# Performance work log

Measured on AMD Instinct MI355X. Metric: run time of the kernel, lower is better.

Reference implementation:

```python
import jax, jax.numpy as jnp
import numpy as np

B, N, M, D0, D, H, KW = 2, 512, 512, 1024, 100, 50, 7
K_SLOPE, X0_SIG = 20.0, 0.5  # LogisticActivation(x0=0.5, k=20), k not trained


def setup_inputs() -> dict:
    key = jax.random.key(0)
    ks = jax.random.split(key, 8)
    s = lambda k, shp: jax.random.normal(k, shp, jnp.float32) * 0.05
    return {
        "x0": jax.random.normal(ks[0], (B, N, D0), jnp.float32),
        "x1": jax.random.normal(ks[1], (B, M, D0), jnp.float32),
        "W_proj": s(ks[2], (D0, D)),
        "b_proj": jnp.zeros((D,), jnp.float32),
        "W_hid": s(ks[3], (2 * D, H)),
        "b_hid": jnp.zeros((H,), jnp.float32),
        "conv_w": s(ks[4], (1, H, KW, KW)),  # OIHW
        "conv_b": jnp.zeros((1,), jnp.float32),
        "theta": jnp.array([0.5], jnp.float32),
        "lambda_": jnp.array([0.3], jnp.float32),
        "gamma": jnp.array([0.2], jnp.float32),
    }


def reference(x0, x1, W_proj, b_proj, W_hid, b_hid, conv_w, conv_b, theta, lambda_, gamma):
    # --- embedding: FullyConnectedEmbed (Linear + ReLU) ---
    e0 = jax.nn.relu(x0 @ W_proj + b_proj)  # [B,N,D]
    e1 = jax.nn.relu(x1 @ W_proj + b_proj)  # [B,M,D]
    # --- contact: broadcast features -> 1x1 conv -> 7x7 conv -> sigmoid ---
    diff = jnp.abs(e0[:, :, None, :] - e1[:, None, :, :])   # [B,N,M,D]
    mul = e0[:, :, None, :] * e1[:, None, :, :]             # [B,N,M,D]
    Z = jnp.concatenate([diff, mul], axis=-1)               # [B,N,M,2D]
    Hh = jax.nn.relu(jnp.einsum('bnmc,ch->bhnm', Z, W_hid) + b_hid[None, :, None, None])
    C = jax.lax.conv_general_dilated(Hh, conv_w, (1, 1), 'SAME')
    C = jax.nn.sigmoid(C + conv_b[None, :, None, None])     # [B,1,N,M]
    # --- weighting matrix W (do_w=True) ---
    i = jnp.arange(N, dtype=jnp.float32)
    j = jnp.arange(M, dtype=jnp.float32)
    a = -jnp.square((i + 1 - (N + 1) / 2) / (-(N + 1) / 2))
    b = -jnp.square((j + 1 - (M + 1) / 2) / (-(M + 1) / 2))
    a = jnp.exp(lambda_ * a)                                 # [N]
    b = jnp.exp(lambda_ * b)                                 # [M]
    W = (1 - theta[0]) * (a[:, None] * b[None, :]) + theta[0]
    yhat = C * W                                             # [B,1,N,M]
    # --- global pooling: mean/var threshold + ratio ---
    mu = jnp.mean(yhat, axis=(1, 2, 3), keepdims=True)
    sigma = jnp.var(yhat, axis=(1, 2, 3), ddof=1, keepdims=True)  # torch.var is unbiased
    Q = jax.nn.relu(yhat - mu - gamma[0] * sigma)
    phat = jnp.sum(Q, axis=(1, 2, 3)) / (jnp.sum(jnp.sign(Q), axis=(1, 2, 3)) + 1)
    # --- LogisticActivation ---
    return jnp.clip(1.0 / (1.0 + jnp.exp(-K_SLOPE * (phat - X0_SIG))), 0.0, 1.0)  # [B]
```

## Files before the change

### kernel.cpp

```cpp
#include <hip/hip_runtime.h>
#include <hip/hip_bf16.h>

static constexpr int Bc   = 2;
static constexpr int Nc   = 512;
static constexpr int Mc   = 512;
static constexpr int D0c  = 1024;
static constexpr int Dc   = 100;
static constexpr int Hc   = 50;
static constexpr long long NMc = (long long)Nc * Mc;

__global__ __launch_bounds__(512) void k_embed(
    const float* __restrict__ x0, const float* __restrict__ x1,
    const float* __restrict__ Wp, const float* __restrict__ bp,
    float* __restrict__ e0, float* __restrict__ e1)
{
  __shared__ float xs[8][1024];
  const int t   = threadIdx.x;
  const int rg0 = blockIdx.x * 8;

  #pragma unroll
  for (int i = 0; i < 4; ++i) {
    const int idx = i*512 + t;
    const int r   = idx >> 8;
    const int c4  = idx & 255;
    const int rgs = rg0 + r;
    const float* src = (rgs < Bc*Nc) ? (x0 + (size_t)rgs * D0c)
                                     : (x1 + (size_t)(rgs - Bc*Nc) * D0c);
    *(float4*)&xs[r][c4*4] = *(const float4*)&src[c4*4];
  }
  __syncthreads();

  const int c = t & 127;
  const int q = t >> 7;
  if (c < Dc) {
    const int row0 = q*2, row1 = q*2 + 1;
    float acc0 = 0.f, acc1 = 0.f;
    for (int k = 0; k < D0c; k += 8) {
      float w[8];
      #pragma unroll
      for (int u = 0; u < 8; ++u) w[u] = Wp[(k+u)*Dc + c];
      const float4 xa0 = *(const float4*)&xs[row0][k];
      const float4 xb0 = *(const float4*)&xs[row0][k+4];
      const float4 xa1 = *(const float4*)&xs[row1][k];
      const float4 xb1 = *(const float4*)&xs[row1][k+4];
      acc0 = fmaf(xa0.x, w[0], acc0); acc1 = fmaf(xa1.x, w[0], acc1);
      acc0 = fmaf(xa0.y, w[1], acc0); acc1 = fmaf(xa1.y, w[1], acc1);
      acc0 = fmaf(xa0.z, w[2], acc0); acc1 = fmaf(xa1.z, w[2], acc1);
      acc0 = fmaf(xa0.w, w[3], acc0); acc1 = fmaf(xa1.w, w[3], acc1);
      acc0 = fmaf(xb0.x, w[4], acc0); acc1 = fmaf(xb1.x, w[4], acc1);
      acc0 = fmaf(xb0.y, w[5], acc0); acc1 = fmaf(xb1.y, w[5], acc1);
      acc0 = fmaf(xb0.z, w[6], acc0); acc1 = fmaf(xb1.z, w[6], acc1);
      acc0 = fmaf(xb0.w, w[7], acc0); acc1 = fmaf(xb1.w, w[7], acc1);
    }
    const float bias = bp[c];
    {
      const int rg = rg0 + row0;
      const float v = fmaxf(acc0 + bias, 0.f);
      if (rg < Bc*Nc) e0[(size_t)rg*Dc + c] = v;
      else            e1[(size_t)(rg - Bc*Nc)*Dc + c] = v;
    }
    {
      const int rg = rg0 + row1;
      const float v = fmaxf(acc1 + bias, 0.f);
      if (rg < Bc*Nc) e0[(size_t)rg*Dc + c] = v;
      else            e1[(size_t)(rg - Bc*Nc)*Dc + c] = v;
    }
  }
}

__global__ __launch_bounds__(320) void k_hh(
    const float* __restrict__ e0, const float* __restrict__ e1,
    const float* __restrict__ Whid, const float* __restrict__ bhid,
    float* __restrict__ hh, int slab_n0, int slabh)
{
  __shared__ float e0T[100][16];
  __shared__ float e1T[100][16];
  const int t   = threadIdx.x;
  const int b   = blockIdx.z;
  const int r0t = blockIdx.y * 16;
  const int m0t = blockIdx.x * 16;

  #pragma unroll
  for (int i = t; i < 1600; i += 320) {
    const int r = i & 15, d = i >> 4;
    const int n = slab_n0 + r0t + r;
    e0T[d][r] = ((unsigned)n < (unsigned)Nc) ? e0[((size_t)(b*Nc + n))*Dc + d] : 0.f;
    e1T[d][r] = e1[((size_t)(b*Mc + m0t + r))*Dc + d];
  }
  __syncthreads();

  const int lane  = t & 63;
  const int hbase = __builtin_amdgcn_readfirstlane((t >> 6) * 10);
  const int r0l   = 2 * (lane >> 3);
  const int m0l   = 2 * (lane & 7);

  float acc[2][2][10];
  #pragma unroll
  for (int i = 0; i < 2; ++i)
    #pragma unroll
    for (int j = 0; j < 2; ++j)
      #pragma unroll
      for (int k = 0; k < 10; ++k) acc[i][j][k] = 0.f;

  const float* __restrict__ wdp = Whid + hbase;
  const float* __restrict__ wmp = Whid + 100*Hc + hbase;

  #pragma unroll 2
  for (int d = 0; d < 100; ++d) {
    const float2 a0 = *(const float2*)&e0T[d][r0l];
    const float2 a1 = *(const float2*)&e1T[d][m0l];
    const float ev0[2] = {a0.x, a0.y};
    const float ev1[2] = {a1.x, a1.y};
    #pragma unroll
    for (int i = 0; i < 2; ++i) {
      #pragma unroll
      for (int j = 0; j < 2; ++j) {
        const float df = fabsf(ev0[i] - ev1[j]);
        const float pm = ev0[i] * ev1[j];
        #pragma unroll
        for (int k = 0; k < 10; ++k)
          acc[i][j][k] = fmaf(df, wdp[d*Hc + k], fmaf(pm, wmp[d*Hc + k], acc[i][j][k]));
      }
    }
  }

  #pragma unroll
  for (int k = 0; k < 10; ++k) {
    const int h = hbase + k;
    const float bh = bhid[h];
    #pragma unroll
    for (int i = 0; i < 2; ++i) {
      const int lr = r0t + r0l + i;
      const int n  = slab_n0 + lr;
      if (lr < slabh && (unsigned)n < (unsigned)Nc) {
        float2 v;
        v.x = fmaxf(acc[i][0][k] + bh, 0.f);
        v.y = fmaxf(acc[i][1][k] + bh, 0.f);
        *(float2*)&hh[(((size_t)(b*Hc + h))*slabh + lr)*Mc + (m0t + m0l)] = v;
      }
    }
  }
}

__global__ __launch_bounds__(256) void k_conv(
    const float* __restrict__ hh, const float* __restrict__ cw,
    const float* __restrict__ cb, const float* __restrict__ theta,
    const float* __restrict__ lam, float* __restrict__ yhat,
    double* __restrict__ gacc, int n_begin, int slabh)
{
  __shared__ float tile[2][38*40];
  __shared__ double red[2][4];
  const int t  = threadIdx.x;
  const int b  = blockIdx.z;
  const int n0 = n_begin + blockIdx.y * 32;
  const int m0 = blockIdx.x * 32;

  const int rr = t >> 3;
  const int c0 = 4 * (t & 7);

  float stg[6];
  auto issue = [&](int h) {
    #pragma unroll
    for (int it = 0; it < 6; ++it) {
      const int idx = it*256 + t;
      float v = 0.f;
      if (idx < 38*38) {
        const int r = idx / 38, c = idx - r*38;
        const int gn = n0 - 3 + r, gm = m0 - 3 + c;
        if ((unsigned)gn < (unsigned)Nc && (unsigned)gm < (unsigned)Mc)
          v = hh[(((size_t)(b*Hc + h))*slabh + (gn - n_begin + 3))*Mc + gm];
      }
      stg[it] = v;
    }
  };
  auto commit = [&](int buf) {
    #pragma unroll
    for (int it = 0; it < 6; ++it) {
      const int idx = it*256 + t;
      if (idx < 38*38) {
        const int r = idx / 38, c = idx - r*38;
        tile[buf][r*40 + c] = stg[it];
      }
    }
  };

  issue(0); commit(0);
  __syncthreads();

  float acc0 = 0.f, acc1 = 0.f, acc2 = 0.f, acc3 = 0.f;
  for (int h = 0; h < Hc; ++h) {
    if (h + 1 < Hc) issue(h + 1);
    const int buf = h & 1;
    const float* __restrict__ cp = cw + h*49;
    #pragma unroll
    for (int dn = 0; dn < 7; ++dn) {
      const float* tp = &tile[buf][(rr+dn)*40 + c0];
      const float4 wa = *(const float4*)tp;
      const float4 wb = *(const float4*)(tp+4);
      const float2 wc = *(const float2*)(tp+8);
      const float w_[10] = {wa.x,wa.y,wa.z,wa.w, wb.x,wb.y,wb.z,wb.w, wc.x,wc.y};
      #pragma unroll
      for (int dm = 0; dm < 7; ++dm) {
        const float wv = cp[dn*7 + dm];
        acc0 = fmaf(w_[dm],   wv, acc0);
        acc1 = fmaf(w_[dm+1], wv, acc1);
        acc2 = fmaf(w_[dm+2], wv, acc2);
        acc3 = fmaf(w_[dm+3], wv, acc3);
      }
    }
    __syncthreads();
    if (h + 1 < Hc) { commit((h+1) & 1); __syncthreads(); }
  }

  const float th  = theta[0];
  const float lm  = lam[0];
  const float cbv = cb[0];
  const int n = n0 + rr;
  const int m = m0 + c0;
  const float half1 = 0.5f * (float)(Nc + 1);
  const float inv   = 1.0f / half1;
  const float ti  = ((float)(n+1) - half1) * inv;
  const float av  = expf(-lm * ti * ti);
  float y[4];
  double s = 0.0, ss = 0.0;
  const float a_[4] = {acc0, acc1, acc2, acc3};
  #pragma unroll
  for (int j = 0; j < 4; ++j) {
    const float tj = ((float)(m+1+j) - half1) * inv;
    const float bv = expf(-lm * tj * tj);
    const float sg = 1.f / (1.f + expf(-(a_[j] + cbv)));
    y[j] = sg * ((1.f - th) * av * bv + th);
    s  += (double)y[j];
    ss += (double)y[j] * (double)y[j];
  }
  float4 yv; yv.x = y[0]; yv.y = y[1]; yv.z = y[2]; yv.w = y[3];
  *(float4*)&yhat[((size_t)(b*Nc + n))*Mc + m] = yv;

  for (int off = 32; off > 0; off >>= 1) {
    s  += __shfl_down(s,  off);
    ss += __shfl_down(ss, off);
  }
  const int wave = t >> 6, lane = t & 63;
  if (lane == 0) { red[0][wave] = s; red[1][wave] = ss; }
  __syncthreads();
  if (t == 0) {
    atomicAdd(&gacc[b*4 + 0], red[0][0] + red[0][1] + red[0][2] + red[0][3]);
    atomicAdd(&gacc[b*4 + 1], red[1][0] + red[1][1] + red[1][2] + red[1][3]);
  }
}

__global__ __launch_bounds__(256) void k_q(
    const float* __restrict__ yhat, double* __restrict__ gacc,
    const float* __restrict__ gamma)
{
  const int tid = blockIdx.x * 256 + threadIdx.x;
  const int b = blockIdx.x >> 8;
  const float4 y = ((const float4*)yhat)[tid];
  const double sum = gacc[b*4 + 0], ssq = gacc[b*4 + 1];
  const double mu  = sum / (double)NMc;
  const double var = (ssq - sum * mu) / ((double)NMc - 1.0);
  const double thr = mu + (double)gamma[0] * var;

  double sq = 0.0; int c = 0;
  double q;
  q = (double)y.x - thr; if (q > 0.0) { sq += q; ++c; }
  q = (double)y.y - thr; if (q > 0.0) { sq += q; ++c; }
  q = (double)y.z - thr; if (q > 0.0) { sq += q; ++c; }
  q = (double)y.w - thr; if (q > 0.0) { sq += q; ++c; }

  for (int off = 32; off > 0; off >>= 1) {
    sq += __shfl_down(sq, off);
    c  += __shfl_down(c,  off);
  }
  __shared__ double sr[4];
  __shared__ int    cr[4];
  const int wave = threadIdx.x >> 6, lane = threadIdx.x & 63;
  if (lane == 0) { sr[wave] = sq; cr[wave] = c; }
  __syncthreads();
  if (threadIdx.x == 0) {
    atomicAdd(&gacc[b*4 + 2], sr[0] + sr[1] + sr[2] + sr[3]);
    atomicAdd(&gacc[b*4 + 3], (double)(cr[0] + cr[1] + cr[2] + cr[3]));
  }
}

__global__ void k_out(const double* __restrict__ gacc, float* __restrict__ out)
{
  const int t = threadIdx.x;
  if (t < Bc) {
    const double phat = gacc[t*4 + 2] / (gacc[t*4 + 3] + 1.0);
    double v = 1.0 / (1.0 + exp(-20.0 * (phat - 0.5)));
    v = fmin(fmax(v, 0.0), 1.0);
    out[t] = (float)v;
  }
}

extern "C" void kernel_launch(void* const* d_in, const int* in_sizes, int n_in,
                              void* d_out, int out_size, void* d_ws, size_t ws_size,
                              hipStream_t stream)
{
  const float* x0 = (const float*)d_in[0];
  const float* x1 = (const float*)d_in[1];
  const float* Wp = (const float*)d_in[2];
  const float* bp = (const float*)d_in[3];
  const float* Wh = (const float*)d_in[4];
  const float* bh = (const float*)d_in[5];
  const float* cw = (const float*)d_in[6];
  const float* cb = (const float*)d_in[7];
  const float* th = (const float*)d_in[8];
  const float* lm = (const float*)d_in[9];
  const float* gm = (const float*)d_in[10];
  float* out = (float*)d_out;
  (void)in_sizes; (void)n_in; (void)out_size;

  int slabrows, nslab;
  if      (ws_size >= (size_t)109232128) { slabrows = 512; nslab = 1; }
  else if (ws_size >= (size_t)56803328)  { slabrows = 256; nslab = 2; }
  else                                    { slabrows = 128; nslab = 4; }
  const int slabh = slabrows + 6;
  const size_t hh_bytes = (size_t)slabh * 204800;

  char* ws = (char*)d_ws;
  float*  e0   = (float*)(ws);
  float*  e1   = (float*)(ws + 409600);
  double* gacc = (double*)(ws + 819200);
  float*  hh   = (float*)(ws + 1048576);
  float*  yhat = (float*)(ws + 1048576 + hh_bytes);

  hipMemsetAsync(gacc, 0, 64, stream);
  k_embed<<<dim3(256), dim3(512), 0, stream>>>(x0, x1, Wp, bp, e0, e1);
  for (int s = 0; s < nslab; ++s) {
    const int n_begin = s * slabrows;
    k_hh  <<<dim3(32, (slabh + 15) / 16, 2), dim3(320), 0, stream>>>(
        e0, e1, Wh, bh, hh, n_begin - 3, slabh);
    k_conv<<<dim3(16, slabrows / 32, 2), dim3(256), 0, stream>>>(
        hh, cw, cb, th, lm, yhat, gacc, n_begin, slabh);
  }
  k_q  <<<dim3(512), dim3(256), 0, stream>>>(yhat, gacc, gm);
  k_out<<<dim3(1),   dim3(64),  0, stream>>>(gacc, out);
}
```

Measured before the change: 343.9 us.

## Compute hidden 1x1 projection with split-bf16 MFMA instead of scalar FMA

Replaces the scalar FP32 k_hh loop with MFMA 16x16x32 bf16 instructions. Precision is kept close to FP32 by splitting both operands into hi and lo bf16 parts and summing three products. A new small kernel pre-splits W_hid into a fragment layout, and each block handles one n row against 32 m columns, going through LDS to transpose output before storing. The cost targeted is the large FP32 FMA count of the pairwise feature projection. In exchange it accepts extra packing ALU work, a small precision loss from dropping the lo*lo term, and a different, finer-grained grid.

```diff
diff --git a/kernel.cpp b/kernel.cpp
--- a/kernel.cpp
+++ b/kernel.cpp
@@ -8,6 +8,9 @@
 static constexpr int Dc   = 100;
 static constexpr int Hc   = 50;
 static constexpr long long NMc = (long long)Nc * Mc;
+
+typedef __attribute__((ext_vector_type(8))) short short8v;
+typedef __attribute__((ext_vector_type(4))) float f32x4;
 
 __global__ __launch_bounds__(512) void k_embed(
     const float* __restrict__ x0, const float* __restrict__ x1,
@@ -68,76 +71,123 @@
   }
 }
 
-__global__ __launch_bounds__(320) void k_hh(
+__global__ __launch_bounds__(64) void k_wsplit(
+    const float* __restrict__ Whid, uint4* __restrict__ wsplit)
+{
+  const int fi = blockIdx.x;
+  const int s  = fi >> 3;
+  const int ht = (fi >> 1) & 3;
+  const int hl = fi & 1;
+  const int lane = threadIdx.x;
+  const int h_loc = lane & 15, g = lane >> 4;
+  const int h = ht*16 + h_loc;
+  uint dw[4] = {0u,0u,0u,0u};
+  #pragma unroll
+  for (int j = 0; j < 8; ++j) {
+    const int p = j >> 2, q = j & 3;
+    const int d = s*16 + g*4 + q;
+    float wv = (h < Hc && d < Dc) ? Whid[(size_t)(p*Dc + d)*Hc + h] : 0.f;
+    const uint bits = __float_as_uint(wv);
+    const uint hi_bits = bits & 0xffff0000u;
+    uint e16;
+    if (hl == 0) e16 = hi_bits >> 16;
+    else {
+      const float lo = wv - __uint_as_float(hi_bits);
+      e16 = __float_as_uint(lo) >> 16;
+    }
+    dw[j >> 1] |= e16 << (16 * (j & 1));
+  }
+  uint4 v; v.x = dw[0]; v.y = dw[1]; v.z = dw[2]; v.w = dw[3];
+  wsplit[fi*64 + lane] = v;
+}
+
+__global__ __launch_bounds__(256) void k_hh(
     const float* __restrict__ e0, const float* __restrict__ e1,
-    const float* __restrict__ Whid, const float* __restrict__ bhid,
+    const uint4* __restrict__ wsplit, const float* __restrict__ bhid,
     float* __restrict__ hh, int slab_n0, int slabh)
 {
-  __shared__ float e0T[100][16];
-  __shared__ float e1T[100][16];
+  const int b  = blockIdx.z;
+  const int lr = blockIdx.y;
+  const int n  = slab_n0 + lr;
+  if ((unsigned)n >= (unsigned)Nc) return;
+
+  __shared__ float e1T[32][112];
+  __shared__ float e0s[112];
+  __shared__ float biasl[64];
+  __shared__ float ldsC[4][2][16][17];
+
   const int t   = threadIdx.x;
-  const int b   = blockIdx.z;
-  const int r0t = blockIdx.y * 16;
-  const int m0t = blockIdx.x * 16;
-
-  #pragma unroll
-  for (int i = t; i < 1600; i += 320) {
-    const int r = i & 15, d = i >> 4;
-    const int n = slab_n0 + r0t + r;
-    e0T[d][r] = ((unsigned)n < (unsigned)Nc) ? e0[((size_t)(b*Nc + n))*Dc + d] : 0.f;
-    e1T[d][r] = e1[((size_t)(b*Mc + m0t + r))*Dc + d];
-  }
-  __syncthreads();
-
-  const int lane  = t & 63;
-  const int hbase = __builtin_amdgcn_readfirstlane((t >> 6) * 10);
-  const int r0l   = 2 * (lane >> 3);
-  const int m0l   = 2 * (lane & 7);
-
-  float acc[2][2][10];
-  #pragma unroll
-  for (int i = 0; i < 2; ++i)
-    #pragma unroll
-    for (int j = 0; j < 2; ++j)
-      #pragma unroll
-      for (int k = 0; k < 10; ++k) acc[i][j][k] = 0.f;
-
-  const float* __restrict__ wdp = Whid + hbase;
-  const float* __restrict__ wmp = Whid + 100*Hc + hbase;
-
-  #pragma unroll 2
-  for (int d = 0; d < 100; ++d) {
-    const float2 a0 = *(const float2*)&e0T[d][r0l];
-    const float2 a1 = *(const float2*)&e1T[d][m0l];
-    const float ev0[2] = {a0.x, a0.y};
-    const float ev1[2] = {a1.x, a1.y};
-    #pragma unroll
-    for (int i = 0; i < 2; ++i) {
-      #pragma unroll
-      for (int j = 0; j < 2; ++j) {
-        const float df = fabsf(ev0[i] - ev1[j]);
-        const float pm = ev0[i] * ev1[j];
-        #pragma unroll
-        for (int k = 0; k < 10; ++k)
-          acc[i][j][k] = fmaf(df, wdp[d*Hc + k], fmaf(pm, wmp[d*Hc + k], acc[i][j][k]));
-      }
-    }
-  }
-
-  #pragma unroll
-  for (int k = 0; k < 10; ++k) {
-    const int h = hbase + k;
-    const float bh = bhid[h];
-    #pragma unroll
-    for (int i = 0; i < 2; ++i) {
-      const int lr = r0t + r0l + i;
-      const int n  = slab_n0 + lr;
-      if (lr < slabh && (unsigned)n < (unsigned)Nc) {
-        float2 v;
-        v.x = fmaxf(acc[i][0][k] + bh, 0.f);
-        v.y = fmaxf(acc[i][1][k] + bh, 0.f);
-        *(float2*)&hh[(((size_t)(b*Hc + h))*slabh + lr)*Mc + (m0t + m0l)] = v;
-      }
+  const int m0b = blockIdx.x * 32;
+
+  for (int i = t; i < 32*112; i += 256) {
+    const int row = i / 112, col = i - row*112;
+    e1T[row][col] = (col < Dc) ? e1[((size_t)(b*Mc + m0b + row))*Dc + col] : 0.f;
+  }
+  if (t < 112) e0s[t] = (t < Dc) ? e0[((size_t)(b*Nc + n))*Dc + t] : 0.f;
+  if (t >= 128 && t < 192) { const int h = t - 128; biasl[h] = (h < Hc) ? bhid[h] : 0.f; }
+  __syncthreads();
+
+  const int w = t >> 6, lane = t & 63;
+  const int cl = lane & 15, g = lane >> 4;
+  const int mt = w >> 1;
+  const int hhalf = w & 1;
+
+  f32x4 c0 = {0.f,0.f,0.f,0.f}, c1 = {0.f,0.f,0.f,0.f};
+
+  union U { uint4 u; short8v v; };
+
+  for (int s = 0; s < 7; ++s) {
+    const int d0 = s*16 + g*4;
+    const float4 E1 = *(const float4*)&e1T[mt*16 + cl][d0];
+    const float4 E0 = *(const float4*)&e0s[d0];
+
+    const float df0 = fabsf(E0.x - E1.x), df1 = fabsf(E0.y - E1.y),
+                df2 = fabsf(E0.z - E1.z), df3 = fabsf(E0.w - E1.w);
+    const float pm0 = E0.x*E1.x, pm1 = E0.y*E1.y,
+                pm2 = E0.z*E1.z, pm3 = E0.w*E1.w;
+
+    #define PK(a,bq) ((__float_as_uint(bq) & 0xffff0000u) | (__float_as_uint(a) >> 16))
+    #define LO(x) ((x) - __uint_as_float(__float_as_uint(x) & 0xffff0000u))
+    U ahi, alo;
+    ahi.u.x = PK(df0, df1); ahi.u.y = PK(df2, df3);
+    ahi.u.z = PK(pm0, pm1); ahi.u.w = PK(pm2, pm3);
+    const float l0 = LO(df0), l1 = LO(df1), l2 = LO(df2), l3 = LO(df3);
+    const float l4 = LO(pm0), l5 = LO(pm1), l6 = LO(pm2), l7 = LO(pm3);
+    alo.u.x = PK(l0, l1); alo.u.y = PK(l2, l3);
+    alo.u.z = PK(l4, l5); alo.u.w = PK(l6, l7);
+    #undef PK
+    #undef LO
+
+    const int ht0 = hhalf*2, ht1 = hhalf*2 + 1;
+    U whi0, wlo0, whi1, wlo1;
+    whi0.u = wsplit[((s*4 + ht0)*2 + 0)*64 + lane];
+    wlo0.u = wsplit[((s*4 + ht0)*2 + 1)*64 + lane];
+    whi1.u = wsplit[((s*4 + ht1)*2 + 0)*64 + lane];
+    wlo1.u = wsplit[((s*4 + ht1)*2 + 1)*64 + lane];
+
+    c0 = __builtin_amdgcn_mfma_f32_16x16x32_bf16(ahi.v, whi0.v, c0, 0, 0, 0);
+    c0 = __builtin_amdgcn_mfma_f32_16x16x32_bf16(alo.v, whi0.v, c0, 0, 0, 0);
+    c0 = __builtin_amdgcn_mfma_f32_16x16x32_bf16(ahi.v, wlo0.v, c0, 0, 0, 0);
+    c1 = __builtin_amdgcn_mfma_f32_16x16x32_bf16(ahi.v, whi1.v, c1, 0, 0, 0);
+    c1 = __builtin_amdgcn_mfma_f32_16x16x32_bf16(alo.v, whi1.v, c1, 0, 0, 0);
+    c1 = __builtin_amdgcn_mfma_f32_16x16x32_bf16(ahi.v, wlo1.v, c1, 0, 0, 0);
+  }
+
+  #pragma unroll
+  for (int r = 0; r < 4; ++r) {
+    ldsC[w][0][cl][g*4 + r] = c0[r];
+    ldsC[w][1][cl][g*4 + r] = c1[r];
+  }
+
+  #pragma unroll
+  for (int pass = 0; pass < 8; ++pass) {
+    const int row   = pass*4 + g;
+    const int tile  = row >> 4, hl2 = row & 15;
+    const int h     = (hhalf*2 + tile)*16 + hl2;
+    if (h < Hc) {
+      float v = ldsC[w][tile][hl2][cl] + biasl[h];
+      v = fmaxf(v, 0.f);
+      hh[(((size_t)(b*Hc + h))*slabh + lr)*Mc + (m0b + mt*16 + cl)] = v;
     }
   }
 }
@@ -323,15 +373,17 @@
   float*  e0   = (float*)(ws);
   float*  e1   = (float*)(ws + 409600);
   double* gacc = (double*)(ws + 819200);
+  uint4*  wsp  = (uint4*)(ws + 884736);
   float*  hh   = (float*)(ws + 1048576);
   float*  yhat = (float*)(ws + 1048576 + hh_bytes);
 
   hipMemsetAsync(gacc, 0, 64, stream);
+  k_wsplit<<<dim3(56), dim3(64), 0, stream>>>(Wh, wsp);
   k_embed<<<dim3(256), dim3(512), 0, stream>>>(x0, x1, Wp, bp, e0, e1);
   for (int s = 0; s < nslab; ++s) {
     const int n_begin = s * slabrows;
-    k_hh  <<<dim3(32, (slabh + 15) / 16, 2), dim3(320), 0, stream>>>(
-        e0, e1, Wh, bh, hh, n_begin - 3, slabh);
+    k_hh  <<<dim3(16, slabh, 2), dim3(256), 0, stream>>>(
+        e0, e1, wsp, bh, hh, n_begin - 3, slabh);
     k_conv<<<dim3(16, slabrows / 32, 2), dim3(256), 0, stream>>>(
         hh, cw, cb, th, lm, yhat, gacc, n_begin, slabh);
   }
```

New measurement: 302.5 us. 1.14x faster.
